# Kernel optimization log

Hardware: AMD Instinct MI355X
Metric: run time of the kernel (lower is better)

The kernel has to match this reference:

```python
import jax, jax.numpy as jnp
import numpy as np

B, NSTEPS = 256, 128
I, H, V = 128, 1024, 1024  # input_size, hidden_size, output_size
SOS = 0


def setup_inputs() -> dict:
    key = jax.random.key(0)
    ks = jax.random.split(key, 9)
    s = 0.02
    return {
        "z": jax.random.normal(ks[0], (B, I), dtype=jnp.float32),
        "inputs": jax.random.randint(ks[1], (NSTEPS, B), 0, V, dtype=jnp.int64),
        "temperature": 10,  # randn() < 10 always -> teacher forcing every step
        "embed_w": jax.random.normal(ks[2], (V, H), dtype=jnp.float32) * s,
        "z2h_w": jax.random.normal(ks[3], (H, I), dtype=jnp.float32) * s,
        "z2h_b": jnp.zeros((H,), dtype=jnp.float32),
        "gru_w_ih": jax.random.normal(ks[4], (3 * H, H + I), dtype=jnp.float32) * s,
        "gru_b_ih": jnp.zeros((3 * H,), dtype=jnp.float32),
        "gru_w_hh": jax.random.normal(ks[5], (3 * H, H), dtype=jnp.float32) * s,
        "gru_b_hh": jnp.zeros((3 * H,), dtype=jnp.float32),
        "out_w": jax.random.normal(ks[6], (V, H + I), dtype=jnp.float32) * s,
        "out_b": jnp.zeros((V,), dtype=jnp.float32),
    }


def _gru_cell(x, h, w_ih, b_ih, w_hh, b_hh):
    # PyTorch GRU cell math
    gi = x @ w_ih.T + b_ih          # [B, 3H]
    gh = h @ w_hh.T + b_hh          # [B, 3H]
    i_r, i_z, i_n = jnp.split(gi, 3, axis=1)
    h_r, h_z, h_n = jnp.split(gh, 3, axis=1)
    r = jax.nn.sigmoid(i_r + h_r)
    zg = jax.nn.sigmoid(i_z + h_z)
    n = jnp.tanh(i_n + r * h_n)
    return (1.0 - zg) * n + zg * h


def reference(z, inputs, temperature, embed_w, z2h_w, z2h_b,
              gru_w_ih, gru_b_ih, gru_w_hh, gru_b_hh, out_w, out_b):
    # hidden init: z2h(z), n_layers=1 -> single [B, H] state
    h0 = z @ z2h_w.T + z2h_b
    tok0 = jnp.full((z.shape[0],), SOS, dtype=inputs.dtype)

    def step(carry, tok_next):
        tok, h = carry
        emb = jax.nn.relu(embed_w[tok])            # [B, H]
        x = jnp.concatenate([emb, z], axis=1)      # [B, H+I]
        h = _gru_cell(x, h, gru_w_ih, gru_b_ih, gru_w_hh, gru_b_hh)
        o = jnp.concatenate([h, z], axis=1) @ out_w.T + out_b  # [B, V]
        # teacher forcing (temperature >> randn always true): next input = inputs[i]
        return (tok_next, h), o

    (_, _), outs = jax.lax.scan(step, (tok0, h0), inputs)  # outs: [NSTEPS, B, V]
    return outs.transpose(1, 0, 2)  # [B, NSTEPS, V]
```

## Files before the change

### kernel.cpp

```cpp
#include <hip/hip_runtime.h>
#include <stdint.h>


#define NSTEP 128

typedef unsigned short u16;
typedef unsigned int u32;
typedef __attribute__((ext_vector_type(8))) short bf16x8;
typedef __attribute__((ext_vector_type(4))) int i32x4;
typedef __attribute__((ext_vector_type(4))) float f32x4;

typedef __attribute__((address_space(3))) void lds_void;
typedef const __attribute__((address_space(1))) void glb_void;
#define GLD16(g, l) __builtin_amdgcn_global_load_lds((glb_void*)(g), (lds_void*)(l), 16, 0, 0)
#define GLD16C(g, l) __builtin_amdgcn_global_load_lds((glb_void*)(g), (lds_void*)(l), 16, 0, 17)
#define CFENCE() asm volatile("" ::: "memory")
#define SCHEDB() __builtin_amdgcn_sched_barrier(0)

#if __has_builtin(__builtin_amdgcn_exp2f)
#define EXP2(x) __builtin_amdgcn_exp2f(x)
#else
#define EXP2(x) exp2f(x)
#endif
#if __has_builtin(__builtin_amdgcn_rcpf)
#define RCP(x) __builtin_amdgcn_rcpf(x)
#else
#define RCP(x) (1.0f / (x))
#endif

__device__ __forceinline__ u16 f2bf(float f) {
    u32 u = __float_as_uint(f);
    u = (u + 0x7FFFu + ((u >> 16) & 1u)) >> 16;
    return (u16)u;
}
__device__ __forceinline__ float fsigmoid(float x) {
    return RCP(1.f + EXP2(x * -1.44269504f));
}
__device__ __forceinline__ float ftanh(float x) {
    x = fminf(fmaxf(x, -18.f), 18.f);
    float t = EXP2(x * 2.88539008f);
    return (t - 1.f) * RCP(t + 1.f);
}

__device__ __forceinline__ void gloadf(float& d, const float* a) {
    asm volatile("global_load_dword %0, %1, off" : "=&v"(d) : "v"(a) : "memory");
}
__device__ __forceinline__ void gloadi4(i32x4& d, const int* a) {
    asm volatile("global_load_dwordx4 %0, %1, off" : "=&v"(d) : "v"(a) : "memory");
}
__device__ __forceinline__ void gstore_short_c(u16* a, u32 v) {
    asm volatile("global_store_short %0, %1, off sc0 sc1" ::"v"(a), "v"(v) : "memory");
}
__device__ __forceinline__ void gstoref(float* a, float v) {
    asm volatile("global_store_dword %0, %1, off" ::"v"(a), "v"(v) : "memory");
}

__global__ void cast_k(const float* __restrict__ src, int ld, int off, int relu,
                       u16* __restrict__ dst, int n) {
    for (int i = blockIdx.x * blockDim.x + threadIdx.x; i < n; i += gridDim.x * blockDim.x) {
        int row = i >> 10, col = i & 1023;
        float v = src[(long)row * ld + off + col];
        if (relu) v = fmaxf(v, 0.f);
        dst[i] = f2bf(v);
    }
}

__global__ void smallgemm_k(const float* __restrict__ z, const float* __restrict__ W,
                            int ldw, int off, const float* __restrict__ bias,
                            const float* __restrict__ bias2, int n2max,
                            float* __restrict__ C, u16* __restrict__ Cbf, int N) {
    int n = blockIdx.x;
    int b = threadIdx.x;
    float acc = bias[n] + ((bias2 && n < n2max) ? bias2[n] : 0.f);
    const float* zr = z + b * 128;
    const float* wr = W + (long)n * ldw + off;
#pragma unroll 8
    for (int k = 0; k < 128; ++k) acc += zr[k] * wr[k];
    C[b * N + n] = acc;
    if (Cbf) Cbf[b * N + n] = f2bf(acc);
}

__global__ __launch_bounds__(256) void egemm_k(const u16* __restrict__ A,
                                               const u16* __restrict__ W,
                                               float* __restrict__ C) {
    __shared__ __align__(16) u16 lds[2][160 * 64];
    int tid = threadIdx.x, lane = tid & 63, wv = tid >> 6;
    int r0 = (blockIdx.x & 31) * 32;
    int n0 = (blockIdx.x >> 5) * 128;

    f32x4 acc[2][2];
#pragma unroll
    for (int m = 0; m < 2; ++m)
#pragma unroll
        for (int n = 0; n < 2; ++n) acc[m][n] = (f32x4){0.f, 0.f, 0.f, 0.f};

    auto stage = [&](int k0, int bufi) {
#pragma unroll
        for (int r = 0; r < 5; ++r) {
            int L = r * 256 + tid;
            int row = L >> 3;
            int c4 = (L & 7) ^ (row & 7);
            const u16* src = (row < 32)
                                 ? A + (long)(r0 + row) * 1024 + k0 + c4 * 8
                                 : W + (long)(n0 + row - 32) * 1024 + k0 + c4 * 8;
            GLD16(src, &lds[bufi][L * 8]);
        }
    };
    stage(0, 0);
    stage(64, 1);
    for (int it = 0; it < 16; ++it) {
        if (it < 15) asm volatile("s_waitcnt vmcnt(5)" ::: "memory");
        else         asm volatile("s_waitcnt vmcnt(0)" ::: "memory");
        __builtin_amdgcn_s_barrier();
        const char* base = (const char*)&lds[it & 1][0];
        bf16x8 af[2][2], bfr[2][2];
#pragma unroll
        for (int ks = 0; ks < 2; ++ks)
#pragma unroll
            for (int q = 0; q < 2; ++q) {
                int kb = ks * 64 + ((lane >> 4) << 4);
                int rowa = q * 16 + (lane & 15);
                af[ks][q] = *(const bf16x8*)(base + rowa * 128 + (kb ^ ((rowa & 7) << 4)));
                int rowb = 32 + wv * 32 + q * 16 + (lane & 15);
                bfr[ks][q] = *(const bf16x8*)(base + rowb * 128 + (kb ^ ((rowb & 7) << 4)));
            }
#pragma unroll
        for (int ks = 0; ks < 2; ++ks)
#pragma unroll
            for (int m = 0; m < 2; ++m)
#pragma unroll
                for (int n = 0; n < 2; ++n)
                    acc[m][n] = __builtin_amdgcn_mfma_f32_16x16x32_bf16(af[ks][m], bfr[ks][n],
                                                                        acc[m][n], 0, 0, 0);
        asm volatile("s_waitcnt lgkmcnt(0)" ::: "memory");
        __builtin_amdgcn_s_barrier();
        if (it + 2 < 16) stage((it + 2) * 64, it & 1);
    }
#pragma unroll
    for (int m = 0; m < 2; ++m)
#pragma unroll
        for (int n = 0; n < 2; ++n)
#pragma unroll
            for (int r = 0; r < 4; ++r) {
                int row = r0 + m * 16 + ((lane >> 4) << 2) + r;
                int col = n0 + wv * 32 + n * 16 + (lane & 15);
                C[(long)row * 3072 + col] = acc[m][n][r];
            }
}

__global__ __launch_bounds__(256, 1) void decoder_k(
    const u16* __restrict__ Whh,
    const u16* __restrict__ Wout,
    const float* __restrict__ E,
    const float* __restrict__ Zih2,
    const float* __restrict__ Zout,
    const float* __restrict__ bhh,
    const int* __restrict__ toks,
    const float* __restrict__ h0f,
    u16* __restrict__ Hx,
    float* __restrict__ out,
    u32* __restrict__ flags) {
    __shared__ __align__(16) char L[163840];
    const int tid = threadIdx.x, lane = tid & 63, wv = tid >> 6;
    const int bid = blockIdx.x;
    const int rB = bid >> 6;
    const int c = bid & 63;

#pragma unroll
    for (int r = 0; r < 8; ++r) {
        int l = r * 256 + tid, row = l >> 7, ck = (l & 127) ^ (row & 15);
        GLD16(Whh + (long)(c * 16 + row) * 1024 + ck * 8, &L[98304 + l * 16]);
    }
#pragma unroll
    for (int r = 0; r < 16; ++r) {
        int l = r * 256 + tid, row = l >> 7, ck = (l & 127) ^ (row & 15);
        GLD16(Whh + (long)((1 + (row >> 4)) * 1024 + c * 16 + (row & 15)) * 1024 + ck * 8,
              &L[l * 16]);
    }
#pragma unroll
    for (int r = 0; r < 8; ++r) {
        int l = r * 256 + tid, row = l >> 7, ck = (l & 127) ^ (row & 15);
        GLD16(Wout + (long)(c * 16 + row) * 1024 + ck * 8, &L[65536 + l * 16]);
    }
    asm volatile("s_waitcnt vmcnt(0)" ::: "memory");
    __builtin_amdgcn_s_barrier();
    bf16x8 w0[32];
#pragma unroll
    for (int it = 0; it < 8; ++it)
#pragma unroll
        for (int ks = 0; ks < 4; ++ks) {
            int row = lane & 15, kc = it * 16 + ks * 4 + (lane >> 4);
            w0[it * 4 + ks] = *(const bf16x8*)(L + 98304 + row * 2048 + ((kc ^ row) << 4));
        }
    asm volatile("s_waitcnt lgkmcnt(0)" ::: "memory");
    __builtin_amdgcn_s_barrier();

    const int bbase = rB * 64 + wv * 16 + ((lane >> 4) << 2);
    const int j = c * 16 + (lane & 15);
    const float bhn = bhh[2048 + j];
    float hprev[4], zi0[4], zi1[4], zi2[4], zo[4];
#pragma unroll
    for (int r = 0; r < 4; ++r) {
        int b = bbase + r;
        hprev[r] = h0f[b * 1024 + j];
        zi0[r] = Zih2[(long)b * 3072 + j];
        zi1[r] = Zih2[(long)b * 3072 + 1024 + j];
        zi2[r] = Zih2[(long)b * 3072 + 2048 + j];
        zo[r] = Zout[b * 1024 + j];
    }

    float ec0[4], ec1[4], ec2[4], en0[4], en1[4], en2[4];
#pragma unroll
    for (int r = 0; r < 4; ++r) {
        const float* eb = E + j;
        gloadf(en0[r], eb);
        gloadf(en1[r], eb + 1024);
        gloadf(en2[r], eb + 2048);
    }

    for (int s = 0; s <= NSTEP; ++s) {
        i32x4 tokv;
        if (s < NSTEP) gloadi4(tokv, toks + s * 256 + bbase);

        const u16* hsrc = Hx + (size_t)(s & 1) * 262144;
        auto stage = [&](int ch) {
            char* dst = L + 98304 + (ch & 3) * 16384;
            int k0 = ch * 128;
#pragma unroll
            for (int r = 0; r < 4; ++r) {
                int l = r * 256 + tid, row = l >> 4, ck = (l & 15) ^ (row & 15);
                GLD16C(hsrc + (long)(rB * 64 + row) * 1024 + k0 + ck * 8, dst + l * 16);
            }
        };
        stage(0);
        stage(1);
        stage(2);
        stage(3);
        CFENCE();

        f32x4 a0 = {0.f, 0.f, 0.f, 0.f}, a1 = a0, a2 = a0, aO = a0;
#pragma unroll
        for (int it = 0; it < 8; ++it) {
            if (it < 5)       asm volatile("s_waitcnt vmcnt(12)" ::: "memory");
            else if (it == 5) asm volatile("s_waitcnt vmcnt(8)" ::: "memory");
            else if (it == 6) asm volatile("s_waitcnt vmcnt(4)" ::: "memory");
            else              asm volatile("s_waitcnt vmcnt(0)" ::: "memory");
            SCHEDB();
            __builtin_amdgcn_s_barrier();
            const char* Ab = L + 98304 + (it & 3) * 16384;
            bf16x8 af[4];
#pragma unroll
            for (int ks = 0; ks < 4; ++ks) {
                int row = wv * 16 + (lane & 15), kc = ks * 4 + (lane >> 4);
                af[ks] = *(const bf16x8*)(Ab + row * 256 + ((kc ^ (row & 15)) << 4));
            }
#pragma unroll
            for (int ks = 0; ks < 4; ++ks)
                a0 = __builtin_amdgcn_mfma_f32_16x16x32_bf16(af[ks], w0[it * 4 + ks], a0, 0, 0, 0);
#pragma unroll
            for (int ks = 0; ks < 4; ++ks) {
                int row = lane & 15, kc = it * 16 + ks * 4 + (lane >> 4);
                bf16x8 wg = *(const bf16x8*)(L + row * 2048 + ((kc ^ row) << 4));
                a1 = __builtin_amdgcn_mfma_f32_16x16x32_bf16(af[ks], wg, a1, 0, 0, 0);
            }
#pragma unroll
            for (int ks = 0; ks < 4; ++ks) {
                int row = 16 + (lane & 15), kc = it * 16 + ks * 4 + (lane >> 4);
                bf16x8 wg = *(const bf16x8*)(L + row * 2048 + ((kc ^ (row & 15)) << 4));
                a2 = __builtin_amdgcn_mfma_f32_16x16x32_bf16(af[ks], wg, a2, 0, 0, 0);
            }
#pragma unroll
            for (int ks = 0; ks < 4; ++ks) {
                int row = lane & 15, kc = it * 16 + ks * 4 + (lane >> 4);
                bf16x8 wo = *(const bf16x8*)(L + 65536 + row * 2048 + ((kc ^ row) << 4));
                aO = __builtin_amdgcn_mfma_f32_16x16x32_bf16(af[ks], wo, aO, 0, 0, 0);
            }
            asm volatile("s_waitcnt lgkmcnt(0)" ::: "memory");
            __builtin_amdgcn_s_barrier();
            if (it < 4) stage(it + 4);
        }
        if (s < NSTEP) {
#pragma unroll
            for (int r = 0; r < 4; ++r) {
                ec0[r] = en0[r];
                ec1[r] = en1[r];
                ec2[r] = en2[r];
            }
        }

        if (s < NSTEP) {
            u16* hdst = Hx + (size_t)((s + 1) & 1) * 262144;
#pragma unroll
            for (int r = 0; r < 4; ++r) {
                float rg = fsigmoid(ec0[r] + zi0[r] + a0[r]);
                float zg = fsigmoid(ec1[r] + zi1[r] + a1[r]);
                float nn = ftanh(ec2[r] + zi2[r] + rg * (a2[r] + bhn));
                float hv = (1.f - zg) * nn + zg * hprev[r];
                hprev[r] = hv;
                gstore_short_c(hdst + (bbase + r) * 1024 + j, (u32)f2bf(hv));
            }
        }
        if (s >= 1) {
#pragma unroll
            for (int r = 0; r < 4; ++r)
                gstoref(out + (long)(bbase + r) * 131072 + (long)(s - 1) * 1024 + j,
                        aO[r] + zo[r]);
        }
        if (s < NSTEP) {
#pragma unroll
            for (int r = 0; r < 4; ++r) {
                const float* eb = E + (long)tokv[r] * 3072 + j;
                gloadf(en0[r], eb);
                gloadf(en1[r], eb + 1024);
                gloadf(en2[r], eb + 2048);
            }
            if (s >= 1) asm volatile("s_waitcnt vmcnt(16)" ::: "memory");
            else        asm volatile("s_waitcnt vmcnt(12)" ::: "memory");
            SCHEDB();
            __builtin_amdgcn_s_barrier();
            if (tid < 64) {
                if (tid == 0)
                    __hip_atomic_store(&flags[bid], (u32)(s + 1), __ATOMIC_RELAXED,
                                       __HIP_MEMORY_SCOPE_AGENT);
                const u32 tgt = (u32)(s + 1);
                const u32* gf = flags + (rB << 6);
                while (true) {
                    u32 v = __hip_atomic_load(&gf[tid], __ATOMIC_RELAXED,
                                              __HIP_MEMORY_SCOPE_AGENT);
                    if (__all(v >= tgt)) break;
                    __builtin_amdgcn_s_sleep(1);
                }
            }
            __builtin_amdgcn_s_barrier();
        }
    }
}

extern "C" void kernel_launch(void* const* d_in, const int* in_sizes, int n_in,
                              void* d_out, int out_size, void* d_ws, size_t ws_size,
                              hipStream_t stream) {
    const float* z = (const float*)d_in[0];
    const int* toks = (const int*)d_in[1];
    const float* embed_w = (const float*)d_in[3];
    const float* z2h_w = (const float*)d_in[4];
    const float* z2h_b = (const float*)d_in[5];
    const float* w_ih = (const float*)d_in[6];
    const float* b_ih = (const float*)d_in[7];
    const float* w_hh = (const float*)d_in[8];
    const float* b_hh = (const float*)d_in[9];
    const float* out_w = (const float*)d_in[10];
    const float* out_b = (const float*)d_in[11];
    float* out = (float*)d_out;

    char* ws = (char*)d_ws;
    size_t off = 0;
    auto alloc = [&](size_t bytes) {
        char* p = ws + off;
        off += (bytes + 255) & ~(size_t)255;
        return p;
    };
    u16* Whh_bf = (u16*)alloc(3072ull * 1024 * 2);
    u16* Wout_bf = (u16*)alloc(1024ull * 1024 * 2);
    u16* Wihh_bf = (u16*)alloc(3072ull * 1024 * 2);
    u16* Emb_bf = (u16*)alloc(1024ull * 1024 * 2);
    float* E = (float*)alloc(1024ull * 3072 * 4);
    float* Zih = (float*)alloc(256ull * 3072 * 4);
    float* Zout = (float*)alloc(256ull * 1024 * 4);
    float* hf = (float*)alloc(256ull * 1024 * 4);
    u16* Hx = (u16*)alloc(2ull * 256 * 1024 * 2);
    u32* flags = (u32*)alloc(1024);

    hipMemsetAsync(flags, 0, 1024, stream);
    cast_k<<<2048, 256, 0, stream>>>(w_hh, 1024, 0, 0, Whh_bf, 3072 * 1024);
    cast_k<<<2048, 256, 0, stream>>>(out_w, 1152, 0, 0, Wout_bf, 1024 * 1024);
    cast_k<<<2048, 256, 0, stream>>>(w_ih, 1152, 0, 0, Wihh_bf, 3072 * 1024);
    cast_k<<<1024, 256, 0, stream>>>(embed_w, 1024, 0, 1, Emb_bf, 1024 * 1024);
    smallgemm_k<<<1024, 256, 0, stream>>>(z, z2h_w, 128, 0, z2h_b, nullptr, 0, hf, Hx, 1024);
    smallgemm_k<<<3072, 256, 0, stream>>>(z, w_ih, 1152, 1024, b_ih, b_hh, 2048, Zih, nullptr, 3072);
    smallgemm_k<<<1024, 256, 0, stream>>>(z, out_w, 1152, 1024, out_b, nullptr, 0, Zout, nullptr, 1024);
    egemm_k<<<768, 256, 0, stream>>>(Emb_bf, Wihh_bf, E);

    decoder_k<<<256, 256, 0, stream>>>(Whh_bf, Wout_bf, E, Zih, Zout, b_hh, toks, hf, Hx, out,
                                       flags);
}
```

Measured before the change: 1.123 ms.

## Keep two gate weight slices in registers, split barrier, widen LDS staging ring

Holds both the reset and update gate weight slices in registers, so only the new-gate and output weights are read from LDS. This frees LDS for a 6-slot staging ring for the hidden state, which lets all chunk prefetches be issued early and drops the per-iteration LDS wait and barrier. The grid barrier is split: each block waits at the end of a step only for the first 32 blocks' flags, and waits for the second half at the start of the next step after issuing the first four chunk loads. The costs are much higher register pressure and subtler ordering between the flag waits and the hidden-state loads.

```diff
diff --git a/kernel.cpp b/kernel.cpp
--- a/kernel.cpp
+++ b/kernel.cpp
@@ -169,30 +169,37 @@
 #pragma unroll
     for (int r = 0; r < 8; ++r) {
         int l = r * 256 + tid, row = l >> 7, ck = (l & 127) ^ (row & 15);
-        GLD16(Whh + (long)(c * 16 + row) * 1024 + ck * 8, &L[98304 + l * 16]);
-    }
-#pragma unroll
-    for (int r = 0; r < 16; ++r) {
-        int l = r * 256 + tid, row = l >> 7, ck = (l & 127) ^ (row & 15);
-        GLD16(Whh + (long)((1 + (row >> 4)) * 1024 + c * 16 + (row & 15)) * 1024 + ck * 8,
-              &L[l * 16]);
+        GLD16(Whh + (long)(c * 16 + row) * 1024 + ck * 8, &L[65536 + l * 16]);
     }
 #pragma unroll
     for (int r = 0; r < 8; ++r) {
         int l = r * 256 + tid, row = l >> 7, ck = (l & 127) ^ (row & 15);
-        GLD16(Wout + (long)(c * 16 + row) * 1024 + ck * 8, &L[65536 + l * 16]);
+        GLD16(Whh + (long)(1024 + c * 16 + row) * 1024 + ck * 8, &L[98304 + l * 16]);
     }
     asm volatile("s_waitcnt vmcnt(0)" ::: "memory");
     __builtin_amdgcn_s_barrier();
-    bf16x8 w0[32];
+    bf16x8 w0[32], w1[32];
 #pragma unroll
     for (int it = 0; it < 8; ++it)
 #pragma unroll
         for (int ks = 0; ks < 4; ++ks) {
             int row = lane & 15, kc = it * 16 + ks * 4 + (lane >> 4);
-            w0[it * 4 + ks] = *(const bf16x8*)(L + 98304 + row * 2048 + ((kc ^ row) << 4));
+            w0[it * 4 + ks] = *(const bf16x8*)(L + 65536 + row * 2048 + ((kc ^ row) << 4));
+            w1[it * 4 + ks] = *(const bf16x8*)(L + 98304 + row * 2048 + ((kc ^ row) << 4));
         }
     asm volatile("s_waitcnt lgkmcnt(0)" ::: "memory");
+    __builtin_amdgcn_s_barrier();
+#pragma unroll
+    for (int r = 0; r < 8; ++r) {
+        int l = r * 256 + tid, row = l >> 7, ck = (l & 127) ^ (row & 15);
+        GLD16(Whh + (long)(2048 + c * 16 + row) * 1024 + ck * 8, &L[l * 16]);
+    }
+#pragma unroll
+    for (int r = 0; r < 8; ++r) {
+        int l = r * 256 + tid, row = l >> 7, ck = (l & 127) ^ (row & 15);
+        GLD16(Wout + (long)(c * 16 + row) * 1024 + ck * 8, &L[32768 + l * 16]);
+    }
+    asm volatile("s_waitcnt vmcnt(0)" ::: "memory");
     __builtin_amdgcn_s_barrier();
 
     const int bbase = rB * 64 + wv * 16 + ((lane >> 4) << 2);
@@ -224,7 +231,7 @@
 
         const u16* hsrc = Hx + (size_t)(s & 1) * 262144;
         auto stage = [&](int ch) {
-            char* dst = L + 98304 + (ch & 3) * 16384;
+            char* dst = L + 65536 + (ch % 6) * 16384;
             int k0 = ch * 128;
 #pragma unroll
             for (int r = 0; r < 4; ++r) {
@@ -238,16 +245,32 @@
         stage(3);
         CFENCE();
 
+        if (s >= 1) {
+            if (tid < 64) {
+                const u32 tgt = (u32)s;
+                const u32* gf = flags + (rB << 6) + 32;
+                while (true) {
+                    u32 v = __hip_atomic_load(gf + (lane & 31), __ATOMIC_RELAXED,
+                                              __HIP_MEMORY_SCOPE_AGENT);
+                    if (__all(v >= tgt)) break;
+                    __builtin_amdgcn_s_sleep(1);
+                }
+            }
+            __builtin_amdgcn_s_barrier();
+        }
+
         f32x4 a0 = {0.f, 0.f, 0.f, 0.f}, a1 = a0, a2 = a0, aO = a0;
 #pragma unroll
         for (int it = 0; it < 8; ++it) {
-            if (it < 5)       asm volatile("s_waitcnt vmcnt(12)" ::: "memory");
+            if (it < 4) stage(it + 4);
+            if (it < 4)       asm volatile("s_waitcnt vmcnt(16)" ::: "memory");
+            else if (it == 4) asm volatile("s_waitcnt vmcnt(12)" ::: "memory");
             else if (it == 5) asm volatile("s_waitcnt vmcnt(8)" ::: "memory");
             else if (it == 6) asm volatile("s_waitcnt vmcnt(4)" ::: "memory");
             else              asm volatile("s_waitcnt vmcnt(0)" ::: "memory");
             SCHEDB();
             __builtin_amdgcn_s_barrier();
-            const char* Ab = L + 98304 + (it & 3) * 16384;
+            const char* Ab = L + 65536 + (it % 6) * 16384;
             bf16x8 af[4];
 #pragma unroll
             for (int ks = 0; ks < 4; ++ks) {
@@ -258,26 +281,20 @@
             for (int ks = 0; ks < 4; ++ks)
                 a0 = __builtin_amdgcn_mfma_f32_16x16x32_bf16(af[ks], w0[it * 4 + ks], a0, 0, 0, 0);
 #pragma unroll
+            for (int ks = 0; ks < 4; ++ks)
+                a1 = __builtin_amdgcn_mfma_f32_16x16x32_bf16(af[ks], w1[it * 4 + ks], a1, 0, 0, 0);
+#pragma unroll
             for (int ks = 0; ks < 4; ++ks) {
                 int row = lane & 15, kc = it * 16 + ks * 4 + (lane >> 4);
                 bf16x8 wg = *(const bf16x8*)(L + row * 2048 + ((kc ^ row) << 4));
-                a1 = __builtin_amdgcn_mfma_f32_16x16x32_bf16(af[ks], wg, a1, 0, 0, 0);
-            }
-#pragma unroll
-            for (int ks = 0; ks < 4; ++ks) {
-                int row = 16 + (lane & 15), kc = it * 16 + ks * 4 + (lane >> 4);
-                bf16x8 wg = *(const bf16x8*)(L + row * 2048 + ((kc ^ (row & 15)) << 4));
                 a2 = __builtin_amdgcn_mfma_f32_16x16x32_bf16(af[ks], wg, a2, 0, 0, 0);
             }
 #pragma unroll
             for (int ks = 0; ks < 4; ++ks) {
                 int row = lane & 15, kc = it * 16 + ks * 4 + (lane >> 4);
-                bf16x8 wo = *(const bf16x8*)(L + 65536 + row * 2048 + ((kc ^ row) << 4));
+                bf16x8 wo = *(const bf16x8*)(L + 32768 + row * 2048 + ((kc ^ row) << 4));
                 aO = __builtin_amdgcn_mfma_f32_16x16x32_bf16(af[ks], wo, aO, 0, 0, 0);
             }
-            asm volatile("s_waitcnt lgkmcnt(0)" ::: "memory");
-            __builtin_amdgcn_s_barrier();
-            if (it < 4) stage(it + 4);
         }
         if (s < NSTEP) {
 #pragma unroll
@@ -318,14 +335,14 @@
             else        asm volatile("s_waitcnt vmcnt(12)" ::: "memory");
             SCHEDB();
             __builtin_amdgcn_s_barrier();
+            if (tid == 0)
+                __hip_atomic_store(&flags[bid], (u32)(s + 1), __ATOMIC_RELAXED,
+                                   __HIP_MEMORY_SCOPE_AGENT);
             if (tid < 64) {
-                if (tid == 0)
-                    __hip_atomic_store(&flags[bid], (u32)(s + 1), __ATOMIC_RELAXED,
-                                       __HIP_MEMORY_SCOPE_AGENT);
                 const u32 tgt = (u32)(s + 1);
                 const u32* gf = flags + (rB << 6);
                 while (true) {
-                    u32 v = __hip_atomic_load(&gf[tid], __ATOMIC_RELAXED,
+                    u32 v = __hip_atomic_load(gf + (lane & 31), __ATOMIC_RELAXED,
                                               __HIP_MEMORY_SCOPE_AGENT);
                     if (__all(v >= tgt)) break;
                     __builtin_amdgcn_s_sleep(1);
```

New measurement: 1.117 ms, median of 2. No clear change (-0.5%).
